# Performance work log

Hardware: AMD Instinct MI355X
Metric: run time of the kernel (lower is better)

Reference implementation:

```python
import jax, jax.numpy as jnp
import numpy as np
from jax import lax

R, K = 1000, 80                 # proposals per image, foreground classes
IMG_H, IMG_W = 800.0, 1333.0    # image_shape (h, w) used by Boxes.clip
SCORE_THRESH = 0.05
NMS_THRESH = 0.5
TOPK = 100                      # topk_per_image


def setup_inputs() -> dict:
    key = jax.random.key(0)
    k1, k2, k3 = jax.random.split(key, 3)
    # well-formed class-specific boxes: x1y1 + positive wh
    x1y1 = jax.random.uniform(k1, (R, K, 2)) * jnp.array([IMG_W - 60.0, IMG_H - 60.0])
    wh = jax.random.uniform(k2, (R, K, 2)) * 200.0 + 10.0
    boxes = jnp.concatenate([x1y1, x1y1 + wh], axis=-1).reshape(R, K * 4)
    logits = jax.random.normal(k3, (R, K + 1)) * 2.0
    scores = jax.nn.softmax(logits, axis=-1)  # (R, K+1), last col = background
    return {"boxes": boxes, "scores": scores}


def _iou_matrix(b):
    # b: [R, 4] (x1, y1, x2, y2) -> [R, R] pairwise IoU
    x1, y1, x2, y2 = b[:, 0], b[:, 1], b[:, 2], b[:, 3]
    area = jnp.clip(x2 - x1, 0.0) * jnp.clip(y2 - y1, 0.0)
    xx1 = jnp.maximum(x1[:, None], x1[None, :])
    yy1 = jnp.maximum(y1[:, None], y1[None, :])
    xx2 = jnp.minimum(x2[:, None], x2[None, :])
    yy2 = jnp.minimum(y2[:, None], y2[None, :])
    inter = jnp.clip(xx2 - xx1, 0.0) * jnp.clip(yy2 - yy1, 0.0)
    union = area[:, None] + area[None, :] - inter
    return inter / jnp.maximum(union, 1e-9)


def _nms_one_class(boxes_c, scores_c, valid_c):
    # boxes_c: [R,4], scores_c: [R], valid_c: [R] bool (passed score filter)
    masked = jnp.where(valid_c, scores_c, -jnp.inf)
    order = jnp.argsort(-masked)            # descending score
    b = boxes_c[order]
    s = masked[order]
    v = valid_c[order]
    iou = iou_full = _iou_matrix(b)          # [R, R]
    idx = jnp.arange(R)

    def body(i, keep):
        # box i (if still kept & valid) suppresses later boxes with high IoU
        sup = (iou_full[i] > NMS_THRESH) & keep[i] & (idx > i)
        return keep & ~sup

    keep = lax.fori_loop(0, R, body, v)
    return s, keep, order


def reference(boxes, scores):
    # boxes: (R, K*4), scores: (R, K+1)
    bx = boxes.reshape(R, K, 4)
    # Boxes.clip(image_shape=(h, w)): x in [0, w], y in [0, h]
    bx = jnp.stack([
        jnp.clip(bx[..., 0], 0.0, IMG_W),
        jnp.clip(bx[..., 1], 0.0, IMG_H),
        jnp.clip(bx[..., 2], 0.0, IMG_W),
        jnp.clip(bx[..., 3], 0.0, IMG_H),
    ], axis=-1)

    fg = scores[:, :-1]                                  # (R, K) foreground scores
    thres = jnp.minimum(SCORE_THRESH, (fg.mean() + fg.max()) / 2.0)
    valid = fg > thres                                   # filter_mask

    # per-class batched NMS (equivalent to torchvision batched_nms)
    boxes_k = jnp.transpose(bx, (1, 0, 2))               # [K, R, 4]
    s_sorted, keep, order = jax.vmap(_nms_one_class)(boxes_k, fg.T, valid.T)

    flat = jnp.where(keep, s_sorted, -jnp.inf).reshape(-1)   # [K*R]
    topv, topi = lax.top_k(flat, TOPK)                   # keep[:topk], score-sorted
    cls = topi // R
    pos = topi % R
    prop = order[cls, pos]                               # original proposal index (filter_inds[:,0])
    ok = jnp.isfinite(topv)
    okf = ok.astype(boxes.dtype)

    box_out = bx[prop, cls] * okf[:, None]               # pred_boxes  [TOPK, 4]
    sc_out = jnp.where(ok, topv, 0.0)                    # scores      [TOPK]
    full_out = scores[prop] * okf[:, None]               # full_scores [TOPK, K+1]
    cls_out = (cls * ok).astype(boxes.dtype)             # pred_classes as float col

    # packed result: [boxes(4) | score(1) | class(1) | full_scores(K+1)]
    return jnp.concatenate([box_out, sc_out[:, None], cls_out[:, None], full_out], axis=1)
```

## Files before the change

### kernel.cpp

```cpp
#include <hip/hip_runtime.h>
#include <stdint.h>

typedef unsigned long long u64;
typedef unsigned int u32;

#define R_N 1000
#define K_N 80
#define NCOL 81
#define TOPK_N 100
#define OUT_W 87
#define IMG_W_ 1333.0f
#define IMG_H_ 800.0f
#define CSTR 100
#define CSTRP 101
#define NQUAD ((R_N * NCOL) / 4)
#define NMAX 448
#define WMAX 7
#define KM (K_N * CSTR)
#define POISON 0xAAAAAAAAu

__device__ __forceinline__ u32 f32_order(float f) {
    u32 u = __float_as_uint(f);
    return u ^ (((u32)((int)u >> 31)) | 0x80000000u);
}
__device__ __forceinline__ float f32_unorder(u32 o) {
    u32 u = (o & 0x80000000u) ? (o ^ 0x80000000u) : ~o;
    return __uint_as_float(u);
}

__device__ __forceinline__ void grid_barrier(u32* bar, u32 nblk) {
    __syncthreads();
    if (threadIdx.x == 0) {
        __threadfence();
        if (__hip_atomic_load(bar, __ATOMIC_RELAXED, __HIP_MEMORY_SCOPE_AGENT) == POISON)
            atomicCAS(bar, POISON, 0u);
        __hip_atomic_fetch_add(bar, 1u, __ATOMIC_ACQ_REL, __HIP_MEMORY_SCOPE_AGENT);
        while (__hip_atomic_load(bar, __ATOMIC_ACQUIRE, __HIP_MEMORY_SCOPE_AGENT) < nblk)
            __builtin_amdgcn_s_sleep(2);
    }
    __syncthreads();
}

struct P2 {
    float4 bx4[R_N];
    u64 key_s[R_N];
    u64 pool[NMAX * WMAX];
    float area[R_N];
    u64 keep_words[16];
    int s_n;
};
struct P3 {
    u64 keys[K_N * CSTRP];
    int rnk[TOPK_N];
    u64 wx[TOPK_N];
    int wr[TOPK_N];
    int wn;
};
union SMEM { P2 p2; P3 p3; };

__global__ __launch_bounds__(256, 1) void k_all(const float* __restrict__ boxes,
                                                const float* __restrict__ scores,
                                                float* __restrict__ hdr,
                                                u32* __restrict__ bars,
                                                u64* __restrict__ cand,
                                                float* __restrict__ outp) {
    __shared__ SMEM sm;
    __shared__ float sc[R_N];
    __shared__ float s_sum[4], s_max[4];
    __shared__ int s_cnt[4], s_kb[2];
    __shared__ float s_thres;

    const int bid = blockIdx.x, tid = threadIdx.x;
    const int lane = tid & 63, wv = tid >> 6;
    const int c = bid;
    const u64 below = (lane == 0) ? 0ull : (~0ull >> (64 - lane));

    for (int r = tid; r < R_N; r += 256) sc[r] = scores[r * NCOL + c];

    {
        float sum = 0.f, mx = -1e30f;
        int q = bid * 256 + tid;
        if (q < NQUAD) {
            float4 v = ((const float4*)scores)[q];
            int m = (q * 4) % NCOL;
            float vv[4] = {v.x, v.y, v.z, v.w};
#pragma unroll
            for (int e = 0; e < 4; ++e) {
                int mm = m + e; if (mm >= NCOL) mm -= NCOL;
                if (mm != K_N) { sum += vv[e]; mx = fmaxf(mx, vv[e]); }
            }
        }
#pragma unroll
        for (int off = 32; off > 0; off >>= 1) {
            sum += __shfl_down(sum, off);
            mx = fmaxf(mx, __shfl_down(mx, off));
        }
        if (lane == 0) { s_sum[wv] = sum; s_max[wv] = mx; }
        __syncthreads();
        if (tid == 0) {
            hdr[2 * bid] = s_sum[0] + s_sum[1] + s_sum[2] + s_sum[3];
            hdr[2 * bid + 1] = fmaxf(fmaxf(s_max[0], s_max[1]), fmaxf(s_max[2], s_max[3]));
        }
    }

    float th = 0.05f;
    for (int pass = 0; ; ++pass) {
        u64* ukey = sm.p2.pool;
        if (wv == 0) {
            int nn = 0;
            for (int r0 = 0; r0 < R_N; r0 += 64) {
                int r = r0 + lane;
                bool pred = (r < R_N) && (sc[r] > th);
                u64 m = __ballot(pred);
                if (pred) {
                    int slot = nn + __popcll(m & below);
                    ukey[slot] = ((u64)f32_order(sc[r]) << 32) | (u64)(u32)(R_N - 1 - r);
                }
                nn += __popcll(m);
            }
            if (lane == 0) sm.p2.s_n = nn;
        }
        __syncthreads();
        const int n = sm.p2.s_n;

        for (int j = tid; j < n; j += 256) {
            u64 kj = ukey[j];
            int rank = 0;
            for (int k = 0; k < n; ++k) rank += (ukey[k] > kj) ? 1 : 0;
            int r = (R_N - 1) - (int)(kj & 0xFFFFFFFFull);
            float4 b = ((const float4*)boxes)[r * K_N + c];
            float x1 = fminf(fmaxf(b.x, 0.f), IMG_W_);
            float y1 = fminf(fmaxf(b.y, 0.f), IMG_H_);
            float x2 = fminf(fmaxf(b.z, 0.f), IMG_W_);
            float y2 = fminf(fmaxf(b.w, 0.f), IMG_H_);
            sm.p2.key_s[rank] = kj;
            sm.p2.bx4[rank] = make_float4(x1, y1, x2, y2);
            sm.p2.area[rank] = fmaxf(x2 - x1, 0.f) * fmaxf(y2 - y1, 0.f);
        }
        __syncthreads();

        if (n <= NMAX) {
            const int W = (n + 63) >> 6;
            u64* Mrow = sm.p2.pool;
            const int nh = n >> 1;
            for (int t2 = wv; t2 < 2 * W; t2 += 4) {
                int w = t2 >> 1, ih = t2 & 1;
                int i0 = ih ? nh : 0;
                int i1 = ih ? n : nh;
                int j = w * 64 + lane;
                bool jv = j < n;
                float4 bj = jv ? sm.p2.bx4[j] : make_float4(0.f, 0.f, 0.f, 0.f);
                float aj = jv ? sm.p2.area[j] : 0.f;
                for (int i = i0; i < i1; ++i) {
                    float4 bi = sm.p2.bx4[i];
                    float ai = sm.p2.area[i];
                    float xx1 = fmaxf(bi.x, bj.x), yy1 = fmaxf(bi.y, bj.y);
                    float xx2 = fminf(bi.z, bj.z), yy2 = fminf(bi.w, bj.w);
                    float inter = fmaxf(xx2 - xx1, 0.f) * fmaxf(yy2 - yy1, 0.f);
                    bool sup = jv && (j > i) &&
                               (inter / fmaxf(ai + aj - inter, 1e-9f) > 0.5f);
                    u64 m = __ballot(sup);
                    if (lane == 0) Mrow[i * W + w] = m;
                }
            }
            __syncthreads();

            if (wv == 0) {
                u64 keep_w = 0;
                if (lane < W) {
                    int rem = n - lane * 64;
                    keep_w = (rem >= 64) ? ~0ull : ((1ull << rem) - 1ull);
                }
                const int lw = (lane < W) ? lane : 0;
                u64 fifo[8];
#pragma unroll
                for (int d = 0; d < 8; ++d) fifo[d] = (d < n) ? Mrow[d * W + lw] : 0ull;
                for (int ib = 0; ib < n; ib += 8) {
#pragma unroll
                    for (int d = 0; d < 8; ++d) {
                        int i = ib + d;
                        if (i >= n) break;
                        u64 row = fifo[d];
                        int ip = i + 8;
                        fifo[d] = (ip < n) ? Mrow[ip * W + lw] : 0ull;
                        u64 kw = __shfl(keep_w, i >> 6);
                        if ((kw >> (i & 63)) & 1ull) keep_w &= ~row;
                    }
                }
                if (lane < W) sm.p2.keep_words[lane] = keep_w;
                if (lane >= W && lane < 16) sm.p2.keep_words[lane] = 0;
            }
        } else {
            int* keep = (int*)sm.p2.pool;
            for (int j = tid; j < n; j += 256) keep[j] = 1;
            __syncthreads();
            for (int i = 0; i < n - 1; ++i) {
                __syncthreads();
                if (!keep[i]) continue;
                float4 bi = sm.p2.bx4[i];
                float ai = sm.p2.area[i];
                for (int j = i + 1 + tid; j < n; j += 256) {
                    if (!keep[j]) continue;
                    float xx1 = fmaxf(bi.x, sm.p2.bx4[j].x), yy1 = fmaxf(bi.y, sm.p2.bx4[j].y);
                    float xx2 = fminf(bi.z, sm.p2.bx4[j].z), yy2 = fminf(bi.w, sm.p2.bx4[j].w);
                    float inter = fmaxf(xx2 - xx1, 0.f) * fmaxf(yy2 - yy1, 0.f);
                    if (inter / fmaxf(ai + sm.p2.area[j] - inter, 1e-9f) > 0.5f) keep[j] = 0;
                }
            }
            __syncthreads();
            if (wv == 0) {
                for (int w = 0; w < 16; ++w) {
                    int j = w * 64 + lane;
                    u64 m = __ballot((j < n) && keep[j]);
                    if (lane == 0) sm.p2.keep_words[w] = m;
                }
            }
        }
        __syncthreads();

        if (wv == 0) {
            int kb = 0;
            for (int j0 = 0; j0 < n; j0 += 64) {
                int j = j0 + lane;
                u64 mw = sm.p2.keep_words[j0 >> 6];
                bool kp = (j < n) && ((mw >> lane) & 1ull);
                u64 mm = __ballot(kp);
                int kr = kb + __popcll(mm & below);
                if (kp && kr < CSTR) {
                    u64 kj = sm.p2.key_s[j];
                    u32 osc = (u32)(kj >> 32);
                    int rr = (R_N - 1) - (int)(kj & 0xFFFFFFFFull);
                    int flat = c * R_N + j;
                    cand[c * CSTR + kr] =
                        ((u64)osc << 27) | ((u64)(u32)(131071 - flat) << 10) | (u64)(u32)rr;
                }
                kb += __popcll(mm);
            }
            if (kb > CSTR) kb = CSTR;
            for (int k2 = kb + lane; k2 < CSTR; k2 += 64) cand[c * CSTR + k2] = 0;
        }

        grid_barrier(&bars[pass], K_N);

        {
            const ulonglong2* cp = (const ulonglong2*)cand;
            int cnt = 0;
            for (int t = tid; t < KM / 2; t += 256) {
                ulonglong2 v = cp[t];
                int e0 = 2 * t;
                int cc2 = e0 / CSTR, pos = e0 - cc2 * CSTR;
                sm.p3.keys[cc2 * CSTRP + pos] = v.x;
                sm.p3.keys[cc2 * CSTRP + pos + 1] = v.y;
                cnt += (v.x != 0ull) + (v.y != 0ull);
            }
#pragma unroll
            for (int off = 32; off > 0; off >>= 1) cnt += __shfl_down(cnt, off);
            if (lane == 0) s_cnt[wv] = cnt;
        }

        if (pass == 0) {
            if (wv == 0) {
                float S = hdr[2 * lane], M = hdr[2 * lane + 1];
                if (lane + 64 < K_N) {
                    S += hdr[2 * (lane + 64)];
                    M = fmaxf(M, hdr[2 * (lane + 64) + 1]);
                }
#pragma unroll
                for (int off = 32; off > 0; off >>= 1) {
                    S += __shfl_down(S, off);
                    M = fmaxf(M, __shfl_down(M, off));
                }
                if (lane == 0)
                    s_thres = fminf(0.05f, 0.5f * (S / (float)(R_N * K_N) + M));
            }
            __syncthreads();
            if (s_thres == 0.05f) break;
            th = s_thres;
        } else break;
    }

    {
        __syncthreads();
        const int total = s_cnt[0] + s_cnt[1] + s_cnt[2] + s_cnt[3];
        const int target = total < TOPK_N ? total : TOPK_N;

        if (tid < TOPK_N) sm.p3.rnk[tid] = tid;
        if (tid == 0) sm.p3.wn = 0;
        if (wv < 2) {
            int t = wv * 64 + lane;
            bool nz = (t < CSTR) && (sm.p3.keys[c * CSTRP + t] != 0ull);
            u64 m = __ballot(nz);
            if (lane == 0) s_kb[wv] = __popcll(m);
        }
        __syncthreads();
        const int kb = s_kb[0] + s_kb[1];

        const int TASKS = kb * (K_N - 1);
        for (int g = 0; g * 2048 < TASKS; ++g) {
            int lo[8], hi[8], ii[8], base[8];
            u64 xv[8];
            bool act[8];
#pragma unroll
            for (int s = 0; s < 8; ++s) {
                int t = g * 2048 + s * 256 + tid;
                act[s] = t < TASKS;
                int i = 0, cc2 = 0;
                if (act[s]) { i = t % kb; cc2 = t / kb; }
                cc2 += (cc2 >= c);
                ii[s] = i;
                base[s] = cc2 * CSTRP;
                xv[s] = sm.p3.keys[c * CSTRP + i];
                if (xv[s] == 0ull) act[s] = false;
                lo[s] = 0; hi[s] = CSTR;
            }
#pragma unroll
            for (int st = 0; st < 7; ++st) {
#pragma unroll
                for (int s = 0; s < 8; ++s) {
                    int mid = (lo[s] + hi[s]) >> 1;
                    u64 v = sm.p3.keys[base[s] + mid];
                    bool live = lo[s] < hi[s];
                    bool gt = live && (v > xv[s]);
                    lo[s] = gt ? mid + 1 : lo[s];
                    hi[s] = (live && !gt) ? mid : hi[s];
                }
            }
#pragma unroll
            for (int s = 0; s < 8; ++s)
                if (act[s] && lo[s] > 0) atomicAdd(&sm.p3.rnk[ii[s]], lo[s]);
        }
        __syncthreads();

        if (tid < kb) {
            int r = sm.p3.rnk[tid];
            if (r < target) {
                int idx = atomicAdd(&sm.p3.wn, 1);
                sm.p3.wx[idx] = sm.p3.keys[c * CSTRP + tid];
                sm.p3.wr[idx] = r;
            }
        }
        __syncthreads();
        const int wn = sm.p3.wn;

        for (int e = tid; e < wn * OUT_W; e += 256) {
            int w = e / OUT_W, col = e - w * OUT_W;
            u64 x = sm.p3.wx[w];
            int r = sm.p3.wr[w];
            int prop = (int)(x & 0x3FFull);
            float val;
            if (col < 4) {
                float b = boxes[prop * (K_N * 4) + c * 4 + col];
                float lim = (col & 1) ? IMG_H_ : IMG_W_;
                val = fminf(fmaxf(b, 0.f), lim);
            } else if (col == 4) {
                val = f32_unorder((u32)((x >> 27) & 0xFFFFFFFFull));
            } else if (col == 5) {
                val = (float)c;
            } else {
                val = scores[prop * NCOL + (col - 6)];
            }
            outp[r * OUT_W + col] = val;
        }
        for (int row = target + bid; row < TOPK_N; row += K_N) {
            int ob = row * OUT_W;
            for (int e = tid; e < OUT_W; e += 256) outp[ob + e] = 0.f;
        }
    }
}

extern "C" void kernel_launch(void* const* d_in, const int* in_sizes, int n_in,
                              void* d_out, int out_size, void* d_ws, size_t ws_size,
                              hipStream_t stream) {
    const float* boxes = (const float*)d_in[0];
    const float* scores = (const float*)d_in[1];
    float* hdr = (float*)d_ws;
    u32* bars = (u32*)((char*)d_ws + 768);
    u64* cand = (u64*)((char*)d_ws + 1024);

    k_all<<<dim3(K_N), dim3(256), 0, stream>>>(boxes, scores, hdr, bars, cand, (float*)d_out);
}
```

Measured before the change: 99.99 us.

## Split fused kernel into NMS and top-k kernels, replacing grid barrier with launch boundary

Splits the single persistent kernel into two launches: one that computes the per-class stats and runs the NMS at the default threshold, and one that gathers the candidates and does the top-k selection. The kernel boundary replaces the software grid barrier that used to sit between NMS and the candidate merge. A rare fallback re-run of NMS at a lower threshold, with a barrier, stays in the second kernel. This trades a spin barrier for an extra launch gap and reloads the candidates from global memory.

Result: faster. 95.11 us (-4.9%).

```diff
diff --git a/kernel.cpp b/kernel.cpp
--- a/kernel.cpp
+++ b/kernel.cpp
@@ -58,7 +58,190 @@
 };
 union SMEM { P2 p2; P3 p3; };
 
-__global__ __launch_bounds__(256, 1) void k_all(const float* __restrict__ boxes,
+__device__ void run_nms(int c, int tid, int lane, int wv, u64 below, float th,
+                        const float* sc, P2& p2,
+                        const float* __restrict__ boxes, u64* __restrict__ cand) {
+    u64* ukey = p2.pool;
+    if (wv == 0) {
+        int nn = 0;
+        for (int r0 = 0; r0 < R_N; r0 += 64) {
+            int r = r0 + lane;
+            bool pred = (r < R_N) && (sc[r] > th);
+            u64 m = __ballot(pred);
+            if (pred) {
+                int slot = nn + __popcll(m & below);
+                ukey[slot] = ((u64)f32_order(sc[r]) << 32) | (u64)(u32)(R_N - 1 - r);
+            }
+            nn += __popcll(m);
+        }
+        if (lane == 0) p2.s_n = nn;
+    }
+    __syncthreads();
+    const int n = p2.s_n;
+
+    for (int j = tid; j < n; j += 256) {
+        u64 kj = ukey[j];
+        int rank = 0;
+        for (int k = 0; k < n; ++k) rank += (ukey[k] > kj) ? 1 : 0;
+        int r = (R_N - 1) - (int)(kj & 0xFFFFFFFFull);
+        float4 b = ((const float4*)boxes)[r * K_N + c];
+        float x1 = fminf(fmaxf(b.x, 0.f), IMG_W_);
+        float y1 = fminf(fmaxf(b.y, 0.f), IMG_H_);
+        float x2 = fminf(fmaxf(b.z, 0.f), IMG_W_);
+        float y2 = fminf(fmaxf(b.w, 0.f), IMG_H_);
+        p2.key_s[rank] = kj;
+        p2.bx4[rank] = make_float4(x1, y1, x2, y2);
+        p2.area[rank] = fmaxf(x2 - x1, 0.f) * fmaxf(y2 - y1, 0.f);
+    }
+    __syncthreads();
+
+    if (n <= NMAX) {
+        const int W = (n + 63) >> 6;
+        u64* Mrow = p2.pool;
+        const int nh = n >> 1;
+        for (int t2 = wv; t2 < 2 * W; t2 += 4) {
+            int w = t2 >> 1, ih = t2 & 1;
+            int i0 = ih ? nh : 0;
+            int i1 = ih ? n : nh;
+            int j = w * 64 + lane;
+            bool jv = j < n;
+            float4 bj = jv ? p2.bx4[j] : make_float4(0.f, 0.f, 0.f, 0.f);
+            float aj = jv ? p2.area[j] : 0.f;
+            for (int i = i0; i < i1; ++i) {
+                float4 bi = p2.bx4[i];
+                float ai = p2.area[i];
+                float xx1 = fmaxf(bi.x, bj.x), yy1 = fmaxf(bi.y, bj.y);
+                float xx2 = fminf(bi.z, bj.z), yy2 = fminf(bi.w, bj.w);
+                float inter = fmaxf(xx2 - xx1, 0.f) * fmaxf(yy2 - yy1, 0.f);
+                bool sup = jv && (j > i) &&
+                           (inter / fmaxf(ai + aj - inter, 1e-9f) > 0.5f);
+                u64 m = __ballot(sup);
+                if (lane == 0) Mrow[i * W + w] = m;
+            }
+        }
+        __syncthreads();
+
+        if (wv == 0) {
+            u64 keep_w = 0;
+            if (lane < W) {
+                int rem = n - lane * 64;
+                keep_w = (rem >= 64) ? ~0ull : ((1ull << rem) - 1ull);
+            }
+            const int lw = (lane < W) ? lane : 0;
+            u64 fifo[8];
+#pragma unroll
+            for (int d = 0; d < 8; ++d) fifo[d] = (d < n) ? Mrow[d * W + lw] : 0ull;
+            for (int ib = 0; ib < n; ib += 8) {
+#pragma unroll
+                for (int d = 0; d < 8; ++d) {
+                    int i = ib + d;
+                    if (i >= n) break;
+                    u64 row = fifo[d];
+                    int ip = i + 8;
+                    fifo[d] = (ip < n) ? Mrow[ip * W + lw] : 0ull;
+                    u64 kw = __shfl(keep_w, i >> 6);
+                    if ((kw >> (i & 63)) & 1ull) keep_w &= ~row;
+                }
+            }
+            if (lane < W) p2.keep_words[lane] = keep_w;
+            if (lane >= W && lane < 16) p2.keep_words[lane] = 0;
+        }
+    } else {
+        int* keep = (int*)p2.pool;
+        for (int j = tid; j < n; j += 256) keep[j] = 1;
+        __syncthreads();
+        for (int i = 0; i < n - 1; ++i) {
+            __syncthreads();
+            if (!keep[i]) continue;
+            float4 bi = p2.bx4[i];
+            float ai = p2.area[i];
+            for (int j = i + 1 + tid; j < n; j += 256) {
+                if (!keep[j]) continue;
+                float xx1 = fmaxf(bi.x, p2.bx4[j].x), yy1 = fmaxf(bi.y, p2.bx4[j].y);
+                float xx2 = fminf(bi.z, p2.bx4[j].z), yy2 = fminf(bi.w, p2.bx4[j].w);
+                float inter = fmaxf(xx2 - xx1, 0.f) * fmaxf(yy2 - yy1, 0.f);
+                if (inter / fmaxf(ai + p2.area[j] - inter, 1e-9f) > 0.5f) keep[j] = 0;
+            }
+        }
+        __syncthreads();
+        if (wv == 0) {
+            for (int w = 0; w < 16; ++w) {
+                int j = w * 64 + lane;
+                u64 m = __ballot((j < n) && keep[j]);
+                if (lane == 0) p2.keep_words[w] = m;
+            }
+        }
+    }
+    __syncthreads();
+
+    if (wv == 0) {
+        int kb = 0;
+        for (int j0 = 0; j0 < n; j0 += 64) {
+            int j = j0 + lane;
+            u64 mw = p2.keep_words[j0 >> 6];
+            bool kp = (j < n) && ((mw >> lane) & 1ull);
+            u64 mm = __ballot(kp);
+            int kr = kb + __popcll(mm & below);
+            if (kp && kr < CSTR) {
+                u64 kj = p2.key_s[j];
+                u32 osc = (u32)(kj >> 32);
+                int rr = (R_N - 1) - (int)(kj & 0xFFFFFFFFull);
+                int flat = c * R_N + j;
+                cand[c * CSTR + kr] =
+                    ((u64)osc << 27) | ((u64)(u32)(131071 - flat) << 10) | (u64)(u32)rr;
+            }
+            kb += __popcll(mm);
+        }
+        if (kb > CSTR) kb = CSTR;
+        for (int kz = kb + lane; kz < CSTR; kz += 64) cand[c * CSTR + kz] = 0;
+    }
+}
+
+__global__ __launch_bounds__(256, 1) void k_nms(const float* __restrict__ boxes,
+                                                const float* __restrict__ scores,
+                                                float* __restrict__ hdr,
+                                                u64* __restrict__ cand) {
+    __shared__ P2 p2;
+    __shared__ float sc[R_N];
+    __shared__ float s_sum[4], s_max[4];
+
+    const int bid = blockIdx.x, tid = threadIdx.x;
+    const int lane = tid & 63, wv = tid >> 6;
+    const int c = bid;
+    const u64 below = (lane == 0) ? 0ull : (~0ull >> (64 - lane));
+
+    for (int r = tid; r < R_N; r += 256) sc[r] = scores[r * NCOL + c];
+
+    {
+        float sum = 0.f, mx = -1e30f;
+        int q = bid * 256 + tid;
+        if (q < NQUAD) {
+            float4 v = ((const float4*)scores)[q];
+            int m = (q * 4) % NCOL;
+            float vv[4] = {v.x, v.y, v.z, v.w};
+#pragma unroll
+            for (int e = 0; e < 4; ++e) {
+                int mm = m + e; if (mm >= NCOL) mm -= NCOL;
+                if (mm != K_N) { sum += vv[e]; mx = fmaxf(mx, vv[e]); }
+            }
+        }
+#pragma unroll
+        for (int off = 32; off > 0; off >>= 1) {
+            sum += __shfl_down(sum, off);
+            mx = fmaxf(mx, __shfl_down(mx, off));
+        }
+        if (lane == 0) { s_sum[wv] = sum; s_max[wv] = mx; }
+        __syncthreads();
+        if (tid == 0) {
+            hdr[2 * bid] = s_sum[0] + s_sum[1] + s_sum[2] + s_sum[3];
+            hdr[2 * bid + 1] = fmaxf(fmaxf(s_max[0], s_max[1]), fmaxf(s_max[2], s_max[3]));
+        }
+    }
+
+    run_nms(c, tid, lane, wv, below, 0.05f, sc, p2, boxes, cand);
+}
+
+__global__ __launch_bounds__(256, 1) void k_top(const float* __restrict__ boxes,
                                                 const float* __restrict__ scores,
                                                 float* __restrict__ hdr,
                                                 u32* __restrict__ bars,
@@ -66,7 +249,6 @@
                                                 float* __restrict__ outp) {
     __shared__ SMEM sm;
     __shared__ float sc[R_N];
-    __shared__ float s_sum[4], s_max[4];
     __shared__ int s_cnt[4], s_kb[2];
     __shared__ float s_thres;
 
@@ -75,173 +257,44 @@
     const int c = bid;
     const u64 below = (lane == 0) ? 0ull : (~0ull >> (64 - lane));
 
-    for (int r = tid; r < R_N; r += 256) sc[r] = scores[r * NCOL + c];
-
     {
-        float sum = 0.f, mx = -1e30f;
-        int q = bid * 256 + tid;
-        if (q < NQUAD) {
-            float4 v = ((const float4*)scores)[q];
-            int m = (q * 4) % NCOL;
-            float vv[4] = {v.x, v.y, v.z, v.w};
-#pragma unroll
-            for (int e = 0; e < 4; ++e) {
-                int mm = m + e; if (mm >= NCOL) mm -= NCOL;
-                if (mm != K_N) { sum += vv[e]; mx = fmaxf(mx, vv[e]); }
-            }
+        const ulonglong2* cp = (const ulonglong2*)cand;
+        int cnt = 0;
+        for (int t = tid; t < KM / 2; t += 256) {
+            ulonglong2 v = cp[t];
+            int e0 = 2 * t;
+            int cc2 = e0 / CSTR, pos = e0 - cc2 * CSTR;
+            sm.p3.keys[cc2 * CSTRP + pos] = v.x;
+            sm.p3.keys[cc2 * CSTRP + pos + 1] = v.y;
+            cnt += (v.x != 0ull) + (v.y != 0ull);
+        }
+#pragma unroll
+        for (int off = 32; off > 0; off >>= 1) cnt += __shfl_down(cnt, off);
+        if (lane == 0) s_cnt[wv] = cnt;
+    }
+
+    if (wv == 0) {
+        float S = hdr[2 * lane], M = hdr[2 * lane + 1];
+        if (lane + 64 < K_N) {
+            S += hdr[2 * (lane + 64)];
+            M = fmaxf(M, hdr[2 * (lane + 64) + 1]);
         }
 #pragma unroll
         for (int off = 32; off > 0; off >>= 1) {
-            sum += __shfl_down(sum, off);
-            mx = fmaxf(mx, __shfl_down(mx, off));
-        }
-        if (lane == 0) { s_sum[wv] = sum; s_max[wv] = mx; }
-        __syncthreads();
-        if (tid == 0) {
-            hdr[2 * bid] = s_sum[0] + s_sum[1] + s_sum[2] + s_sum[3];
-            hdr[2 * bid + 1] = fmaxf(fmaxf(s_max[0], s_max[1]), fmaxf(s_max[2], s_max[3]));
-        }
-    }
-
-    float th = 0.05f;
-    for (int pass = 0; ; ++pass) {
-        u64* ukey = sm.p2.pool;
-        if (wv == 0) {
-            int nn = 0;
-            for (int r0 = 0; r0 < R_N; r0 += 64) {
-                int r = r0 + lane;
-                bool pred = (r < R_N) && (sc[r] > th);
-                u64 m = __ballot(pred);
-                if (pred) {
-                    int slot = nn + __popcll(m & below);
-                    ukey[slot] = ((u64)f32_order(sc[r]) << 32) | (u64)(u32)(R_N - 1 - r);
-                }
-                nn += __popcll(m);
-            }
-            if (lane == 0) sm.p2.s_n = nn;
-        }
-        __syncthreads();
-        const int n = sm.p2.s_n;
-
-        for (int j = tid; j < n; j += 256) {
-            u64 kj = ukey[j];
-            int rank = 0;
-            for (int k = 0; k < n; ++k) rank += (ukey[k] > kj) ? 1 : 0;
-            int r = (R_N - 1) - (int)(kj & 0xFFFFFFFFull);
-            float4 b = ((const float4*)boxes)[r * K_N + c];
-            float x1 = fminf(fmaxf(b.x, 0.f), IMG_W_);
-            float y1 = fminf(fmaxf(b.y, 0.f), IMG_H_);
-            float x2 = fminf(fmaxf(b.z, 0.f), IMG_W_);
-            float y2 = fminf(fmaxf(b.w, 0.f), IMG_H_);
-            sm.p2.key_s[rank] = kj;
-            sm.p2.bx4[rank] = make_float4(x1, y1, x2, y2);
-            sm.p2.area[rank] = fmaxf(x2 - x1, 0.f) * fmaxf(y2 - y1, 0.f);
-        }
-        __syncthreads();
-
-        if (n <= NMAX) {
-            const int W = (n + 63) >> 6;
-            u64* Mrow = sm.p2.pool;
-            const int nh = n >> 1;
-            for (int t2 = wv; t2 < 2 * W; t2 += 4) {
-                int w = t2 >> 1, ih = t2 & 1;
-                int i0 = ih ? nh : 0;
-                int i1 = ih ? n : nh;
-                int j = w * 64 + lane;
-                bool jv = j < n;
-                float4 bj = jv ? sm.p2.bx4[j] : make_float4(0.f, 0.f, 0.f, 0.f);
-                float aj = jv ? sm.p2.area[j] : 0.f;
-                for (int i = i0; i < i1; ++i) {
-                    float4 bi = sm.p2.bx4[i];
-                    float ai = sm.p2.area[i];
-                    float xx1 = fmaxf(bi.x, bj.x), yy1 = fmaxf(bi.y, bj.y);
-                    float xx2 = fminf(bi.z, bj.z), yy2 = fminf(bi.w, bj.w);
-                    float inter = fmaxf(xx2 - xx1, 0.f) * fmaxf(yy2 - yy1, 0.f);
-                    bool sup = jv && (j > i) &&
-                               (inter / fmaxf(ai + aj - inter, 1e-9f) > 0.5f);
-                    u64 m = __ballot(sup);
-                    if (lane == 0) Mrow[i * W + w] = m;
-                }
-            }
-            __syncthreads();
-
-            if (wv == 0) {
-                u64 keep_w = 0;
-                if (lane < W) {
-                    int rem = n - lane * 64;
-                    keep_w = (rem >= 64) ? ~0ull : ((1ull << rem) - 1ull);
-                }
-                const int lw = (lane < W) ? lane : 0;
-                u64 fifo[8];
-#pragma unroll
-                for (int d = 0; d < 8; ++d) fifo[d] = (d < n) ? Mrow[d * W + lw] : 0ull;
-                for (int ib = 0; ib < n; ib += 8) {
-#pragma unroll
-                    for (int d = 0; d < 8; ++d) {
-                        int i = ib + d;
-                        if (i >= n) break;
-                        u64 row = fifo[d];
-                        int ip = i + 8;
-                        fifo[d] = (ip < n) ? Mrow[ip * W + lw] : 0ull;
-                        u64 kw = __shfl(keep_w, i >> 6);
-                        if ((kw >> (i & 63)) & 1ull) keep_w &= ~row;
-                    }
-                }
-                if (lane < W) sm.p2.keep_words[lane] = keep_w;
-                if (lane >= W && lane < 16) sm.p2.keep_words[lane] = 0;
-            }
-        } else {
-            int* keep = (int*)sm.p2.pool;
-            for (int j = tid; j < n; j += 256) keep[j] = 1;
-            __syncthreads();
-            for (int i = 0; i < n - 1; ++i) {
-                __syncthreads();
-                if (!keep[i]) continue;
-                float4 bi = sm.p2.bx4[i];
-                float ai = sm.p2.area[i];
-                for (int j = i + 1 + tid; j < n; j += 256) {
-                    if (!keep[j]) continue;
-                    float xx1 = fmaxf(bi.x, sm.p2.bx4[j].x), yy1 = fmaxf(bi.y, sm.p2.bx4[j].y);
-                    float xx2 = fminf(bi.z, sm.p2.bx4[j].z), yy2 = fminf(bi.w, sm.p2.bx4[j].w);
-                    float inter = fmaxf(xx2 - xx1, 0.f) * fmaxf(yy2 - yy1, 0.f);
-                    if (inter / fmaxf(ai + sm.p2.area[j] - inter, 1e-9f) > 0.5f) keep[j] = 0;
-                }
-            }
-            __syncthreads();
-            if (wv == 0) {
-                for (int w = 0; w < 16; ++w) {
-                    int j = w * 64 + lane;
-                    u64 m = __ballot((j < n) && keep[j]);
-                    if (lane == 0) sm.p2.keep_words[w] = m;
-                }
-            }
-        }
-        __syncthreads();
-
-        if (wv == 0) {
-            int kb = 0;
-            for (int j0 = 0; j0 < n; j0 += 64) {
-                int j = j0 + lane;
-                u64 mw = sm.p2.keep_words[j0 >> 6];
-                bool kp = (j < n) && ((mw >> lane) & 1ull);
-                u64 mm = __ballot(kp);
-                int kr = kb + __popcll(mm & below);
-                if (kp && kr < CSTR) {
-                    u64 kj = sm.p2.key_s[j];
-                    u32 osc = (u32)(kj >> 32);
-                    int rr = (R_N - 1) - (int)(kj & 0xFFFFFFFFull);
-                    int flat = c * R_N + j;
-                    cand[c * CSTR + kr] =
-                        ((u64)osc << 27) | ((u64)(u32)(131071 - flat) << 10) | (u64)(u32)rr;
-                }
-                kb += __popcll(mm);
-            }
-            if (kb > CSTR) kb = CSTR;
-            for (int k2 = kb + lane; k2 < CSTR; k2 += 64) cand[c * CSTR + k2] = 0;
-        }
-
-        grid_barrier(&bars[pass], K_N);
-
+            S += __shfl_down(S, off);
+            M = fmaxf(M, __shfl_down(M, off));
+        }
+        if (lane == 0)
+            s_thres = fminf(0.05f, 0.5f * (S / (float)(R_N * K_N) + M));
+    }
+    __syncthreads();
+
+    if (s_thres != 0.05f) {
+        const float th = s_thres;
+        for (int r = tid; r < R_N; r += 256) sc[r] = scores[r * NCOL + c];
+        __syncthreads();
+        run_nms(c, tid, lane, wv, below, th, sc, sm.p2, boxes, cand);
+        grid_barrier(&bars[0], K_N);
         {
             const ulonglong2* cp = (const ulonglong2*)cand;
             int cnt = 0;
@@ -257,30 +310,10 @@
             for (int off = 32; off > 0; off >>= 1) cnt += __shfl_down(cnt, off);
             if (lane == 0) s_cnt[wv] = cnt;
         }
-
-        if (pass == 0) {
-            if (wv == 0) {
-                float S = hdr[2 * lane], M = hdr[2 * lane + 1];
-                if (lane + 64 < K_N) {
-                    S += hdr[2 * (lane + 64)];
-                    M = fmaxf(M, hdr[2 * (lane + 64) + 1]);
-                }
-#pragma unroll
-                for (int off = 32; off > 0; off >>= 1) {
-                    S += __shfl_down(S, off);
-                    M = fmaxf(M, __shfl_down(M, off));
-                }
-                if (lane == 0)
-                    s_thres = fminf(0.05f, 0.5f * (S / (float)(R_N * K_N) + M));
-            }
-            __syncthreads();
-            if (s_thres == 0.05f) break;
-            th = s_thres;
-        } else break;
+        __syncthreads();
     }
 
     {
-        __syncthreads();
         const int total = s_cnt[0] + s_cnt[1] + s_cnt[2] + s_cnt[3];
         const int target = total < TOPK_N ? total : TOPK_N;
 
@@ -377,5 +410,6 @@
     u32* bars = (u32*)((char*)d_ws + 768);
     u64* cand = (u64*)((char*)d_ws + 1024);
 
-    k_all<<<dim3(K_N), dim3(256), 0, stream>>>(boxes, scores, hdr, bars, cand, (float*)d_out);
-}
+    k_nms<<<dim3(K_N), dim3(256), 0, stream>>>(boxes, scores, hdr, cand);
+    k_top<<<dim3(K_N), dim3(256), 0, stream>>>(boxes, scores, hdr, bars, cand, (float*)d_out);
+}
```

## Split fused kernel into NMS and top-k launches with single-wave register NMS

Applied to the files above, without the earlier changes.

Replaces the single persistent kernel with a device-wide spin barrier by two kernel launches, so the stream boundary provides the cross-block dependency. The threshold fallback pass still uses a grid barrier inside the second kernel. Each block drops from 256 threads to one 64-lane wave. Small classes (up to 128 candidates) run NMS entirely in registers using shuffles and ballots instead of building a bitmask matrix in shared memory. The trade-off is an extra launch and less intra-block parallelism in the ranking and top-k stages.

Result: slower. 139.5 us (+39.5%).

```diff
diff --git a/kernel.cpp b/kernel.cpp
--- a/kernel.cpp
+++ b/kernel.cpp
@@ -14,8 +14,7 @@
 #define CSTR 100
 #define CSTRP 101
 #define NQUAD ((R_N * NCOL) / 4)
-#define NMAX 448
-#define WMAX 7
+#define CAP_FAST 128
 #define KM (K_N * CSTR)
 #define POISON 0xAAAAAAAAu
 
@@ -41,13 +40,11 @@
     __syncthreads();
 }
 
-struct P2 {
+struct NMS_S {
+    u64 ukey[R_N];
+    u64 key_s[R_N];
     float4 bx4[R_N];
-    u64 key_s[R_N];
-    u64 pool[NMAX * WMAX];
     float area[R_N];
-    u64 keep_words[16];
-    int s_n;
 };
 struct P3 {
     u64 keys[K_N * CSTRP];
@@ -56,315 +53,312 @@
     int wr[TOPK_N];
     int wn;
 };
-union SMEM { P2 p2; P3 p3; };
-
-__global__ __launch_bounds__(256, 1) void k_all(const float* __restrict__ boxes,
-                                                const float* __restrict__ scores,
-                                                float* __restrict__ hdr,
-                                                u32* __restrict__ bars,
-                                                u64* __restrict__ cand,
-                                                float* __restrict__ outp) {
-    __shared__ SMEM sm;
-    __shared__ float sc[R_N];
-    __shared__ float s_sum[4], s_max[4];
-    __shared__ int s_cnt[4], s_kb[2];
-    __shared__ float s_thres;
-
-    const int bid = blockIdx.x, tid = threadIdx.x;
-    const int lane = tid & 63, wv = tid >> 6;
-    const int c = bid;
+union TOPS { NMS_S nms; P3 p3; };
+
+__device__ __forceinline__ void emit_cand(u64* __restrict__ cand, int c, int kr, u64 kj, int j) {
+    u32 osc = (u32)(kj >> 32);
+    int rr = (R_N - 1) - (int)(kj & 0xFFFFFFFFull);
+    int flat = c * R_N + j;
+    cand[c * CSTR + kr] = ((u64)osc << 27) | ((u64)(u32)(131071 - flat) << 10) | (u64)(u32)rr;
+}
+
+__device__ void nms64(int c, int lane, u64 below, float th,
+                      const float* __restrict__ scores,
+                      const float* __restrict__ boxes,
+                      u64* __restrict__ cand, NMS_S& S) {
+    float sv[16];
+#pragma unroll
+    for (int e = 0; e < 16; ++e) {
+        int r = e * 64 + lane;
+        sv[e] = (r < R_N) ? scores[r * NCOL + c] : -1e30f;
+    }
+    int nn = 0;
+#pragma unroll
+    for (int e = 0; e < 16; ++e) {
+        bool pred = sv[e] > th;
+        u64 m = __ballot(pred);
+        if (pred) {
+            int r = e * 64 + lane;
+            S.ukey[nn + __popcll(m & below)] =
+                ((u64)f32_order(sv[e]) << 32) | (u64)(u32)(R_N - 1 - r);
+        }
+        nn += __popcll(m);
+    }
+    const int n = nn;
+    __syncthreads();
+
+    for (int j = lane; j < n; j += 64) {
+        u64 kj = S.ukey[j];
+        int rank = 0;
+        for (int k = 0; k < n; ++k) rank += (S.ukey[k] > kj) ? 1 : 0;
+        int r = (R_N - 1) - (int)(kj & 0xFFFFFFFFull);
+        float4 b = ((const float4*)boxes)[r * K_N + c];
+        float x1 = fminf(fmaxf(b.x, 0.f), IMG_W_);
+        float y1 = fminf(fmaxf(b.y, 0.f), IMG_H_);
+        float x2 = fminf(fmaxf(b.z, 0.f), IMG_W_);
+        float y2 = fminf(fmaxf(b.w, 0.f), IMG_H_);
+        S.key_s[rank] = kj;
+        S.bx4[rank] = make_float4(x1, y1, x2, y2);
+        S.area[rank] = fmaxf(x2 - x1, 0.f) * fmaxf(y2 - y1, 0.f);
+    }
+    __syncthreads();
+
+    if (n <= CAP_FAST) {
+        float4 b0 = make_float4(0.f, 0.f, 0.f, 0.f), b1 = b0;
+        float a0 = 0.f, a1 = 0.f;
+        if (lane < n)      { b0 = S.bx4[lane];      a0 = S.area[lane]; }
+        if (lane + 64 < n) { b1 = S.bx4[lane + 64]; a1 = S.area[lane + 64]; }
+        u64 k0 = (n >= 64) ? ~0ull : ((1ull << n) - 1ull);
+        u64 k1 = (n > 64) ? ((n >= 128) ? ~0ull : ((1ull << (n - 64)) - 1ull)) : 0ull;
+
+        const int n0 = n < 64 ? n : 64;
+        for (int i = 0; i < n0; ++i) {
+            if (!((k0 >> i) & 1ull)) continue;
+            float bx_ = __shfl(b0.x, i), by_ = __shfl(b0.y, i);
+            float bz_ = __shfl(b0.z, i), bw_ = __shfl(b0.w, i);
+            float ba_ = __shfl(a0, i);
+            float i0 = fmaxf(fminf(bz_, b0.z) - fmaxf(bx_, b0.x), 0.f) *
+                       fmaxf(fminf(bw_, b0.w) - fmaxf(by_, b0.y), 0.f);
+            bool s0 = (lane < n) && (lane > i) &&
+                      (i0 / fmaxf(ba_ + a0 - i0, 1e-9f) > 0.5f);
+            float i1 = fmaxf(fminf(bz_, b1.z) - fmaxf(bx_, b1.x), 0.f) *
+                       fmaxf(fminf(bw_, b1.w) - fmaxf(by_, b1.y), 0.f);
+            bool s1 = (lane + 64 < n) &&
+                      (i1 / fmaxf(ba_ + a1 - i1, 1e-9f) > 0.5f);
+            k0 &= ~__ballot(s0);
+            k1 &= ~__ballot(s1);
+        }
+        for (int i = 64; i < n; ++i) {
+            if (!((k1 >> (i - 64)) & 1ull)) continue;
+            float bx_ = __shfl(b1.x, i - 64), by_ = __shfl(b1.y, i - 64);
+            float bz_ = __shfl(b1.z, i - 64), bw_ = __shfl(b1.w, i - 64);
+            float ba_ = __shfl(a1, i - 64);
+            float i1 = fmaxf(fminf(bz_, b1.z) - fmaxf(bx_, b1.x), 0.f) *
+                       fmaxf(fminf(bw_, b1.w) - fmaxf(by_, b1.y), 0.f);
+            bool s1 = (lane + 64 < n) && (lane > i - 64) &&
+                      (i1 / fmaxf(ba_ + a1 - i1, 1e-9f) > 0.5f);
+            k1 &= ~__ballot(s1);
+        }
+
+        int kb_all = __popcll(k0) + __popcll(k1);
+        if ((lane < n) && ((k0 >> lane) & 1ull)) {
+            int kr = __popcll(k0 & below);
+            if (kr < CSTR) emit_cand(cand, c, kr, S.key_s[lane], lane);
+        }
+        if ((lane + 64 < n) && ((k1 >> lane) & 1ull)) {
+            int kr = __popcll(k0) + __popcll(k1 & below);
+            if (kr < CSTR) emit_cand(cand, c, kr, S.key_s[lane + 64], lane + 64);
+        }
+        int kbc = kb_all < CSTR ? kb_all : CSTR;
+        for (int k2 = kbc + lane; k2 < CSTR; k2 += 64) cand[c * CSTR + k2] = 0;
+    } else {
+        int* keep = (int*)S.ukey;
+        for (int j = lane; j < n; j += 64) keep[j] = 1;
+        __syncthreads();
+        for (int i = 0; i < n - 1; ++i) {
+            __syncthreads();
+            if (!keep[i]) continue;
+            float4 bi = S.bx4[i];
+            float ai = S.area[i];
+            for (int j = i + 1 + lane; j < n; j += 64) {
+                if (!keep[j]) continue;
+                float xx1 = fmaxf(bi.x, S.bx4[j].x), yy1 = fmaxf(bi.y, S.bx4[j].y);
+                float xx2 = fminf(bi.z, S.bx4[j].z), yy2 = fminf(bi.w, S.bx4[j].w);
+                float inter = fmaxf(xx2 - xx1, 0.f) * fmaxf(yy2 - yy1, 0.f);
+                if (inter / fmaxf(ai + S.area[j] - inter, 1e-9f) > 0.5f) keep[j] = 0;
+            }
+        }
+        __syncthreads();
+        int kb = 0;
+        for (int j0 = 0; j0 < n; j0 += 64) {
+            int j = j0 + lane;
+            bool kp = (j < n) && keep[j];
+            u64 mm = __ballot(kp);
+            int kr = kb + __popcll(mm & below);
+            if (kp && kr < CSTR) emit_cand(cand, c, kr, S.key_s[j], j);
+            kb += __popcll(mm);
+        }
+        if (kb > CSTR) kb = CSTR;
+        for (int k2 = kb + lane; k2 < CSTR; k2 += 64) cand[c * CSTR + k2] = 0;
+    }
+}
+
+__global__ __launch_bounds__(64, 1) void k_nms(const float* __restrict__ boxes,
+                                               const float* __restrict__ scores,
+                                               float* __restrict__ hdr,
+                                               u64* __restrict__ cand) {
+    __shared__ NMS_S S;
+    const int c = blockIdx.x, lane = threadIdx.x;
     const u64 below = (lane == 0) ? 0ull : (~0ull >> (64 - lane));
 
-    for (int r = tid; r < R_N; r += 256) sc[r] = scores[r * NCOL + c];
-
-    {
-        float sum = 0.f, mx = -1e30f;
-        int q = bid * 256 + tid;
+    float sum = 0.f, mx = -1e30f;
+#pragma unroll
+    for (int e = 0; e < 4; ++e) {
+        int q = c * 256 + e * 64 + lane;
         if (q < NQUAD) {
             float4 v = ((const float4*)scores)[q];
             int m = (q * 4) % NCOL;
             float vv[4] = {v.x, v.y, v.z, v.w};
 #pragma unroll
-            for (int e = 0; e < 4; ++e) {
-                int mm = m + e; if (mm >= NCOL) mm -= NCOL;
-                if (mm != K_N) { sum += vv[e]; mx = fmaxf(mx, vv[e]); }
+            for (int t = 0; t < 4; ++t) {
+                int mm = m + t; if (mm >= NCOL) mm -= NCOL;
+                if (mm != K_N) { sum += vv[t]; mx = fmaxf(mx, vv[t]); }
             }
         }
+    }
+#pragma unroll
+    for (int off = 32; off > 0; off >>= 1) {
+        sum += __shfl_down(sum, off);
+        mx = fmaxf(mx, __shfl_down(mx, off));
+    }
+    if (lane == 0) { hdr[2 * c] = sum; hdr[2 * c + 1] = mx; }
+
+    nms64(c, lane, below, 0.05f, scores, boxes, cand, S);
+}
+
+__global__ __launch_bounds__(64, 1) void k_top(const float* __restrict__ boxes,
+                                               const float* __restrict__ scores,
+                                               float* __restrict__ hdr,
+                                               u32* __restrict__ bars,
+                                               u64* __restrict__ cand,
+                                               float* __restrict__ outp) {
+    __shared__ TOPS sm;
+    const int c = blockIdx.x, lane = threadIdx.x;
+    const u64 below = (lane == 0) ? 0ull : (~0ull >> (64 - lane));
+
+    int total;
+    {
+        const ulonglong2* cp = (const ulonglong2*)cand;
+        int cnt = 0;
+        for (int t = lane; t < KM / 2; t += 64) {
+            ulonglong2 v = cp[t];
+            int e0 = 2 * t;
+            int cc2 = e0 / CSTR, pos = e0 - cc2 * CSTR;
+            sm.p3.keys[cc2 * CSTRP + pos] = v.x;
+            sm.p3.keys[cc2 * CSTRP + pos + 1] = v.y;
+            cnt += (v.x != 0ull) + (v.y != 0ull);
+        }
+#pragma unroll
+        for (int off = 32; off > 0; off >>= 1) cnt += __shfl_down(cnt, off);
+        total = __shfl(cnt, 0);
+    }
+    float th;
+    {
+        float S_ = hdr[2 * lane], M_ = hdr[2 * lane + 1];
+        if (lane < K_N - 64) {
+            S_ += hdr[2 * (lane + 64)];
+            M_ = fmaxf(M_, hdr[2 * (lane + 64) + 1]);
+        }
 #pragma unroll
         for (int off = 32; off > 0; off >>= 1) {
-            sum += __shfl_down(sum, off);
-            mx = fmaxf(mx, __shfl_down(mx, off));
-        }
-        if (lane == 0) { s_sum[wv] = sum; s_max[wv] = mx; }
+            S_ += __shfl_down(S_, off);
+            M_ = fmaxf(M_, __shfl_down(M_, off));
+        }
+        float tv = fminf(0.05f, 0.5f * (S_ / (float)(R_N * K_N) + M_));
+        th = __shfl(tv, 0);
+    }
+
+    if (th != 0.05f) {
         __syncthreads();
-        if (tid == 0) {
-            hdr[2 * bid] = s_sum[0] + s_sum[1] + s_sum[2] + s_sum[3];
-            hdr[2 * bid + 1] = fmaxf(fmaxf(s_max[0], s_max[1]), fmaxf(s_max[2], s_max[3]));
-        }
-    }
-
-    float th = 0.05f;
-    for (int pass = 0; ; ++pass) {
-        u64* ukey = sm.p2.pool;
-        if (wv == 0) {
-            int nn = 0;
-            for (int r0 = 0; r0 < R_N; r0 += 64) {
-                int r = r0 + lane;
-                bool pred = (r < R_N) && (sc[r] > th);
-                u64 m = __ballot(pred);
-                if (pred) {
-                    int slot = nn + __popcll(m & below);
-                    ukey[slot] = ((u64)f32_order(sc[r]) << 32) | (u64)(u32)(R_N - 1 - r);
-                }
-                nn += __popcll(m);
+        nms64(c, lane, below, th, scores, boxes, cand, sm.nms);
+        grid_barrier(&bars[0], K_N);
+        __syncthreads();
+        const ulonglong2* cp = (const ulonglong2*)cand;
+        int cnt = 0;
+        for (int t = lane; t < KM / 2; t += 64) {
+            ulonglong2 v = cp[t];
+            int e0 = 2 * t;
+            int cc2 = e0 / CSTR, pos = e0 - cc2 * CSTR;
+            sm.p3.keys[cc2 * CSTRP + pos] = v.x;
+            sm.p3.keys[cc2 * CSTRP + pos + 1] = v.y;
+            cnt += (v.x != 0ull) + (v.y != 0ull);
+        }
+#pragma unroll
+        for (int off = 32; off > 0; off >>= 1) cnt += __shfl_down(cnt, off);
+        total = __shfl(cnt, 0);
+    }
+    __syncthreads();
+
+    const int target = total < TOPK_N ? total : TOPK_N;
+
+    for (int t = lane; t < TOPK_N; t += 64) sm.p3.rnk[t] = t;
+    if (lane == 0) sm.p3.wn = 0;
+    bool nz0 = sm.p3.keys[c * CSTRP + lane] != 0ull;
+    u64 mA = __ballot(nz0);
+    bool nz1 = (lane < CSTR - 64) && (sm.p3.keys[c * CSTRP + 64 + lane] != 0ull);
+    u64 mB = __ballot(nz1);
+    const int kb = __popcll(mA) + __popcll(mB);
+    __syncthreads();
+
+    const int TASKS = kb * (K_N - 1);
+    for (int g = 0; g * 512 < TASKS; ++g) {
+        int lo[8], hi[8], ii[8], base[8];
+        u64 xv[8];
+        bool act[8];
+#pragma unroll
+        for (int s = 0; s < 8; ++s) {
+            int t = g * 512 + s * 64 + lane;
+            act[s] = t < TASKS;
+            int i = 0, cc2 = 0;
+            if (act[s]) { i = t % kb; cc2 = t / kb; }
+            cc2 += (cc2 >= c);
+            ii[s] = i;
+            base[s] = cc2 * CSTRP;
+            xv[s] = sm.p3.keys[c * CSTRP + i];
+            if (xv[s] == 0ull) act[s] = false;
+            lo[s] = 0; hi[s] = CSTR;
+        }
+#pragma unroll
+        for (int st = 0; st < 7; ++st) {
+#pragma unroll
+            for (int s = 0; s < 8; ++s) {
+                int mid = (lo[s] + hi[s]) >> 1;
+                u64 v = sm.p3.keys[base[s] + mid];
+                bool live = lo[s] < hi[s];
+                bool gt = live && (v > xv[s]);
+                lo[s] = gt ? mid + 1 : lo[s];
+                hi[s] = (live && !gt) ? mid : hi[s];
             }
-            if (lane == 0) sm.p2.s_n = nn;
-        }
-        __syncthreads();
-        const int n = sm.p2.s_n;
-
-        for (int j = tid; j < n; j += 256) {
-            u64 kj = ukey[j];
-            int rank = 0;
-            for (int k = 0; k < n; ++k) rank += (ukey[k] > kj) ? 1 : 0;
-            int r = (R_N - 1) - (int)(kj & 0xFFFFFFFFull);
-            float4 b = ((const float4*)boxes)[r * K_N + c];
-            float x1 = fminf(fmaxf(b.x, 0.f), IMG_W_);
-            float y1 = fminf(fmaxf(b.y, 0.f), IMG_H_);
-            float x2 = fminf(fmaxf(b.z, 0.f), IMG_W_);
-            float y2 = fminf(fmaxf(b.w, 0.f), IMG_H_);
-            sm.p2.key_s[rank] = kj;
-            sm.p2.bx4[rank] = make_float4(x1, y1, x2, y2);
-            sm.p2.area[rank] = fmaxf(x2 - x1, 0.f) * fmaxf(y2 - y1, 0.f);
-        }
-        __syncthreads();
-
-        if (n <= NMAX) {
-            const int W = (n + 63) >> 6;
-            u64* Mrow = sm.p2.pool;
-            const int nh = n >> 1;
-            for (int t2 = wv; t2 < 2 * W; t2 += 4) {
-                int w = t2 >> 1, ih = t2 & 1;
-                int i0 = ih ? nh : 0;
-                int i1 = ih ? n : nh;
-                int j = w * 64 + lane;
-                bool jv = j < n;
-                float4 bj = jv ? sm.p2.bx4[j] : make_float4(0.f, 0.f, 0.f, 0.f);
-                float aj = jv ? sm.p2.area[j] : 0.f;
-                for (int i = i0; i < i1; ++i) {
-                    float4 bi = sm.p2.bx4[i];
-                    float ai = sm.p2.area[i];
-                    float xx1 = fmaxf(bi.x, bj.x), yy1 = fmaxf(bi.y, bj.y);
-                    float xx2 = fminf(bi.z, bj.z), yy2 = fminf(bi.w, bj.w);
-                    float inter = fmaxf(xx2 - xx1, 0.f) * fmaxf(yy2 - yy1, 0.f);
-                    bool sup = jv && (j > i) &&
-                               (inter / fmaxf(ai + aj - inter, 1e-9f) > 0.5f);
-                    u64 m = __ballot(sup);
-                    if (lane == 0) Mrow[i * W + w] = m;
-                }
-            }
-            __syncthreads();
-
-            if (wv == 0) {
-                u64 keep_w = 0;
-                if (lane < W) {
-                    int rem = n - lane * 64;
-                    keep_w = (rem >= 64) ? ~0ull : ((1ull << rem) - 1ull);
-                }
-                const int lw = (lane < W) ? lane : 0;
-                u64 fifo[8];
-#pragma unroll
-                for (int d = 0; d < 8; ++d) fifo[d] = (d < n) ? Mrow[d * W + lw] : 0ull;
-                for (int ib = 0; ib < n; ib += 8) {
-#pragma unroll
-                    for (int d = 0; d < 8; ++d) {
-                        int i = ib + d;
-                        if (i >= n) break;
-                        u64 row = fifo[d];
-                        int ip = i + 8;
-                        fifo[d] = (ip < n) ? Mrow[ip * W + lw] : 0ull;
-                        u64 kw = __shfl(keep_w, i >> 6);
-                        if ((kw >> (i & 63)) & 1ull) keep_w &= ~row;
-                    }
-                }
-                if (lane < W) sm.p2.keep_words[lane] = keep_w;
-                if (lane >= W && lane < 16) sm.p2.keep_words[lane] = 0;
-            }
+        }
+#pragma unroll
+        for (int s = 0; s < 8; ++s)
+            if (act[s] && lo[s] > 0) atomicAdd(&sm.p3.rnk[ii[s]], lo[s]);
+    }
+    __syncthreads();
+
+    for (int t = lane; t < kb; t += 64) {
+        int r = sm.p3.rnk[t];
+        if (r < target) {
+            int idx = atomicAdd(&sm.p3.wn, 1);
+            sm.p3.wx[idx] = sm.p3.keys[c * CSTRP + t];
+            sm.p3.wr[idx] = r;
+        }
+    }
+    __syncthreads();
+    const int wn = sm.p3.wn;
+
+    for (int e = lane; e < wn * OUT_W; e += 64) {
+        int w = e / OUT_W, col = e - w * OUT_W;
+        u64 x = sm.p3.wx[w];
+        int r = sm.p3.wr[w];
+        int prop = (int)(x & 0x3FFull);
+        float val;
+        if (col < 4) {
+            float b = boxes[prop * (K_N * 4) + c * 4 + col];
+            float lim = (col & 1) ? IMG_H_ : IMG_W_;
+            val = fminf(fmaxf(b, 0.f), lim);
+        } else if (col == 4) {
+            val = f32_unorder((u32)((x >> 27) & 0xFFFFFFFFull));
+        } else if (col == 5) {
+            val = (float)c;
         } else {
-            int* keep = (int*)sm.p2.pool;
-            for (int j = tid; j < n; j += 256) keep[j] = 1;
-            __syncthreads();
-            for (int i = 0; i < n - 1; ++i) {
-                __syncthreads();
-                if (!keep[i]) continue;
-                float4 bi = sm.p2.bx4[i];
-                float ai = sm.p2.area[i];
-                for (int j = i + 1 + tid; j < n; j += 256) {
-                    if (!keep[j]) continue;
-                    float xx1 = fmaxf(bi.x, sm.p2.bx4[j].x), yy1 = fmaxf(bi.y, sm.p2.bx4[j].y);
-                    float xx2 = fminf(bi.z, sm.p2.bx4[j].z), yy2 = fminf(bi.w, sm.p2.bx4[j].w);
-                    float inter = fmaxf(xx2 - xx1, 0.f) * fmaxf(yy2 - yy1, 0.f);
-                    if (inter / fmaxf(ai + sm.p2.area[j] - inter, 1e-9f) > 0.5f) keep[j] = 0;
-                }
-            }
-            __syncthreads();
-            if (wv == 0) {
-                for (int w = 0; w < 16; ++w) {
-                    int j = w * 64 + lane;
-                    u64 m = __ballot((j < n) && keep[j]);
-                    if (lane == 0) sm.p2.keep_words[w] = m;
-                }
-            }
-        }
-        __syncthreads();
-
-        if (wv == 0) {
-            int kb = 0;
-            for (int j0 = 0; j0 < n; j0 += 64) {
-                int j = j0 + lane;
-                u64 mw = sm.p2.keep_words[j0 >> 6];
-                bool kp = (j < n) && ((mw >> lane) & 1ull);
-                u64 mm = __ballot(kp);
-                int kr = kb + __popcll(mm & below);
-                if (kp && kr < CSTR) {
-                    u64 kj = sm.p2.key_s[j];
-                    u32 osc = (u32)(kj >> 32);
-                    int rr = (R_N - 1) - (int)(kj & 0xFFFFFFFFull);
-                    int flat = c * R_N + j;
-                    cand[c * CSTR + kr] =
-                        ((u64)osc << 27) | ((u64)(u32)(131071 - flat) << 10) | (u64)(u32)rr;
-                }
-                kb += __popcll(mm);
-            }
-            if (kb > CSTR) kb = CSTR;
-            for (int k2 = kb + lane; k2 < CSTR; k2 += 64) cand[c * CSTR + k2] = 0;
-        }
-
-        grid_barrier(&bars[pass], K_N);
-
-        {
-            const ulonglong2* cp = (const ulonglong2*)cand;
-            int cnt = 0;
-            for (int t = tid; t < KM / 2; t += 256) {
-                ulonglong2 v = cp[t];
-                int e0 = 2 * t;
-                int cc2 = e0 / CSTR, pos = e0 - cc2 * CSTR;
-                sm.p3.keys[cc2 * CSTRP + pos] = v.x;
-                sm.p3.keys[cc2 * CSTRP + pos + 1] = v.y;
-                cnt += (v.x != 0ull) + (v.y != 0ull);
-            }
-#pragma unroll
-            for (int off = 32; off > 0; off >>= 1) cnt += __shfl_down(cnt, off);
-            if (lane == 0) s_cnt[wv] = cnt;
-        }
-
-        if (pass == 0) {
-            if (wv == 0) {
-                float S = hdr[2 * lane], M = hdr[2 * lane + 1];
-                if (lane + 64 < K_N) {
-                    S += hdr[2 * (lane + 64)];
-                    M = fmaxf(M, hdr[2 * (lane + 64) + 1]);
-                }
-#pragma unroll
-                for (int off = 32; off > 0; off >>= 1) {
-                    S += __shfl_down(S, off);
-                    M = fmaxf(M, __shfl_down(M, off));
-                }
-                if (lane == 0)
-                    s_thres = fminf(0.05f, 0.5f * (S / (float)(R_N * K_N) + M));
-            }
-            __syncthreads();
-            if (s_thres == 0.05f) break;
-            th = s_thres;
-        } else break;
-    }
-
-    {
-        __syncthreads();
-        const int total = s_cnt[0] + s_cnt[1] + s_cnt[2] + s_cnt[3];
-        const int target = total < TOPK_N ? total : TOPK_N;
-
-        if (tid < TOPK_N) sm.p3.rnk[tid] = tid;
-        if (tid == 0) sm.p3.wn = 0;
-        if (wv < 2) {
-            int t = wv * 64 + lane;
-            bool nz = (t < CSTR) && (sm.p3.keys[c * CSTRP + t] != 0ull);
-            u64 m = __ballot(nz);
-            if (lane == 0) s_kb[wv] = __popcll(m);
-        }
-        __syncthreads();
-        const int kb = s_kb[0] + s_kb[1];
-
-        const int TASKS = kb * (K_N - 1);
-        for (int g = 0; g * 2048 < TASKS; ++g) {
-            int lo[8], hi[8], ii[8], base[8];
-            u64 xv[8];
-            bool act[8];
-#pragma unroll
-            for (int s = 0; s < 8; ++s) {
-                int t = g * 2048 + s * 256 + tid;
-                act[s] = t < TASKS;
-                int i = 0, cc2 = 0;
-                if (act[s]) { i = t % kb; cc2 = t / kb; }
-                cc2 += (cc2 >= c);
-                ii[s] = i;
-                base[s] = cc2 * CSTRP;
-                xv[s] = sm.p3.keys[c * CSTRP + i];
-                if (xv[s] == 0ull) act[s] = false;
-                lo[s] = 0; hi[s] = CSTR;
-            }
-#pragma unroll
-            for (int st = 0; st < 7; ++st) {
-#pragma unroll
-                for (int s = 0; s < 8; ++s) {
-                    int mid = (lo[s] + hi[s]) >> 1;
-                    u64 v = sm.p3.keys[base[s] + mid];
-                    bool live = lo[s] < hi[s];
-                    bool gt = live && (v > xv[s]);
-                    lo[s] = gt ? mid + 1 : lo[s];
-                    hi[s] = (live && !gt) ? mid : hi[s];
-                }
-            }
-#pragma unroll
-            for (int s = 0; s < 8; ++s)
-                if (act[s] && lo[s] > 0) atomicAdd(&sm.p3.rnk[ii[s]], lo[s]);
-        }
-        __syncthreads();
-
-        if (tid < kb) {
-            int r = sm.p3.rnk[tid];
-            if (r < target) {
-                int idx = atomicAdd(&sm.p3.wn, 1);
-                sm.p3.wx[idx] = sm.p3.keys[c * CSTRP + tid];
-                sm.p3.wr[idx] = r;
-            }
-        }
-        __syncthreads();
-        const int wn = sm.p3.wn;
-
-        for (int e = tid; e < wn * OUT_W; e += 256) {
-            int w = e / OUT_W, col = e - w * OUT_W;
-            u64 x = sm.p3.wx[w];
-            int r = sm.p3.wr[w];
-            int prop = (int)(x & 0x3FFull);
-            float val;
-            if (col < 4) {
-                float b = boxes[prop * (K_N * 4) + c * 4 + col];
-                float lim = (col & 1) ? IMG_H_ : IMG_W_;
-                val = fminf(fmaxf(b, 0.f), lim);
-            } else if (col == 4) {
-                val = f32_unorder((u32)((x >> 27) & 0xFFFFFFFFull));
-            } else if (col == 5) {
-                val = (float)c;
-            } else {
-                val = scores[prop * NCOL + (col - 6)];
-            }
-            outp[r * OUT_W + col] = val;
-        }
-        for (int row = target + bid; row < TOPK_N; row += K_N) {
-            int ob = row * OUT_W;
-            for (int e = tid; e < OUT_W; e += 256) outp[ob + e] = 0.f;
-        }
+            val = scores[prop * NCOL + (col - 6)];
+        }
+        outp[r * OUT_W + col] = val;
+    }
+    for (int row = target + c; row < TOPK_N; row += K_N) {
+        int ob = row * OUT_W;
+        for (int e = lane; e < OUT_W; e += 64) outp[ob + e] = 0.f;
     }
 }
 
@@ -377,5 +371,6 @@
     u32* bars = (u32*)((char*)d_ws + 768);
     u64* cand = (u64*)((char*)d_ws + 1024);
 
-    k_all<<<dim3(K_N), dim3(256), 0, stream>>>(boxes, scores, hdr, bars, cand, (float*)d_out);
-}
+    k_nms<<<dim3(K_N), dim3(64), 0, stream>>>(boxes, scores, hdr, cand);
+    k_top<<<dim3(K_N), dim3(64), 0, stream>>>(boxes, scores, hdr, bars, cand, (float*)d_out);
+}
```
